# Kernel optimization log

Hardware: AMD Instinct MI355X
Metric: run time of the kernel (lower is better)

The kernel has to match this reference:

```python
import jax, jax.numpy as jnp
import numpy as np

M_MOL = 8192      # number of molecules
A_ATOMS = 32      # atoms per molecule (uniform ragged groups)
N_FEAT = 128      # schnet n_atom_basis


def setup_inputs() -> dict:
    key = jax.random.key(0)
    sr = jax.random.normal(key, (M_MOL * A_ATOMS, N_FEAT), dtype=jnp.float32)
    # idx_m: sorted molecule index per atom, uniform group sizes
    idx_m = jnp.repeat(jnp.arange(M_MOL, dtype=jnp.int32), A_ATOMS)
    return {"scalar_representation": sr, "idx_m": idx_m}


def reference(scalar_representation, idx_m):
    # maxm = int(idx_m[-1]) + 1 in the torch code; groups are uniform here so
    # torch.split over bincount == a simple reshape into [M, A, F].
    maxm = int(idx_m[-1]) + 1
    n_atoms = scalar_representation.shape[0]
    a = n_atoms // maxm
    sr = scalar_representation.reshape(maxm, a, -1)          # [M, A, F]
    # per-molecule correlation (Gram) matrix: c = sr @ sr.T
    c = jnp.einsum('maf,mbf->mab', sr, sr)                    # [M, A, A]
    # eigvalsh returns ascending eigenvalues; torch code takes [0] (smallest)
    eigvals = jnp.linalg.eigvalsh(c)                          # [M, A]
    return eigvals[:, 0]                                      # [M]
```

## Files before the change

### kernel.cpp

```cpp
#include <hip/hip_runtime.h>
#include <hip/hip_bf16.h>

#define DEVINL __device__ __forceinline__

typedef __attribute__((ext_vector_type(8))) short short8;
typedef __attribute__((ext_vector_type(4))) float f32x4;

DEVINL float rcp_f(float x) { return __builtin_amdgcn_rcpf(x); }

#define LDS_FENCE() __asm__ volatile("" ::: "memory")

template<int CTRL>
DEVINL float dpp_mov(float x) {
  return __int_as_float(__builtin_amdgcn_update_dpp(
      0, __float_as_int(x), CTRL, 0xF, 0xF, true));
}
DEVINL float group_sum(float x) {
  x += dpp_mov<0xB1>(x);
  x += dpp_mov<0x4E>(x);
  x += dpp_mov<0x141>(x);
  x += dpp_mov<0x140>(x);
  return x;
}
DEVINL float group_min(float x) {
  x = fminf(x, dpp_mov<0xB1>(x));
  x = fminf(x, dpp_mov<0x4E>(x));
  x = fminf(x, dpp_mov<0x141>(x));
  x = fminf(x, dpp_mov<0x140>(x));
  return x;
}
DEVINL float group_max(float x) {
  x = fmaxf(x, dpp_mov<0xB1>(x));
  x = fmaxf(x, dpp_mov<0x4E>(x));
  x = fmaxf(x, dpp_mov<0x141>(x));
  x = fmaxf(x, dpp_mov<0x140>(x));
  return x;
}

DEVINL short bf_hi(float f, float& rem) {
  unsigned u = __float_as_uint(f);
  unsigned rh = (u + 0x8000u) >> 16;
  rem = f - __uint_as_float(rh << 16);
  return (short)rh;
}
DEVINL short bf_of(float f) {
  return (short)((__float_as_uint(f) + 0x8000u) >> 16);
}
DEVINL void cvt_hilo(float4 fa, float4 fb, short8& h, short8& lo) {
  float rm;
  h[0] = bf_hi(fa.x, rm); lo[0] = bf_of(rm);
  h[1] = bf_hi(fa.y, rm); lo[1] = bf_of(rm);
  h[2] = bf_hi(fa.z, rm); lo[2] = bf_of(rm);
  h[3] = bf_hi(fa.w, rm); lo[3] = bf_of(rm);
  h[4] = bf_hi(fb.x, rm); lo[4] = bf_of(rm);
  h[5] = bf_hi(fb.y, rm); lo[5] = bf_of(rm);
  h[6] = bf_hi(fb.z, rm); lo[6] = bf_of(rm);
  h[7] = bf_hi(fb.w, rm); lo[7] = bf_of(rm);
}
DEVINL f32x4 mfma_bf16(short8 a, short8 b, f32x4 c) {
  return __builtin_amdgcn_mfma_f32_16x16x32_bf16(a, b, c, 0, 0, 0);
}

template<int K>
DEVINL void house_step(float (&r0)[32], float (&r1)[32], int l, int lane,
                       float* vbuf, float* pbuf, float* dbuf, float* ebuf) {
  constexpr int C0 = (K + 1) / 4;

  float xm0, xm1;
  if constexpr (K < 15) xm0 = (l > K) ? r0[K] : 0.0f;
  else                  xm0 = 0.0f;
  if constexpr (K < 16) xm1 = r1[K];
  else                  xm1 = (l > K - 16) ? r1[K] : 0.0f;

  float xsrc = (K + 1 < 16) ? xm0 : xm1;
  float x0 = __shfl(xsrc, (lane & 48) + ((K + 1) & 15), 64);
  float nn = group_sum(xm0 * xm0 + xm1 * xm1);
  float alpha = -copysignf(sqrtf(nn), x0);
  float denom = nn - alpha * x0;
  float beta = (denom > 1e-20f) ? rcp_f(denom) : 0.0f;

  float v0, v1;
  if constexpr (K + 1 < 16) {
    v0 = xm0 - ((l == K + 1) ? alpha : 0.0f);
    v1 = xm1;
  } else {
    v0 = 0.0f;
    v1 = xm1 - ((l == K + 1 - 16) ? alpha : 0.0f);
  }
  vbuf[l] = v0; vbuf[l + 16] = v1;
  LDS_FENCE();

  float4 vc[8];
  #pragma unroll
  for (int c = C0; c < 8; ++c) vc[c] = *(const float4*)(vbuf + 4 * c);

  float p0 = 0.0f;
  if constexpr (K < 15) {
    float a0 = 0.0f, a1 = 0.0f;
    #pragma unroll
    for (int c = C0; c < 8; ++c) {
      a0 = fmaf(r0[4 * c + 0], vc[c].x, a0); a1 = fmaf(r0[4 * c + 1], vc[c].y, a1);
      a0 = fmaf(r0[4 * c + 2], vc[c].z, a0); a1 = fmaf(r0[4 * c + 3], vc[c].w, a1);
    }
    p0 = a0 + a1;
  }
  float b0 = 0.0f, b1 = 0.0f;
  #pragma unroll
  for (int c = C0; c < 8; ++c) {
    b0 = fmaf(r1[4 * c + 0], vc[c].x, b0); b1 = fmaf(r1[4 * c + 1], vc[c].y, b1);
    b0 = fmaf(r1[4 * c + 2], vc[c].z, b0); b1 = fmaf(r1[4 * c + 3], vc[c].w, b1);
  }
  float p1 = b0 + b1;

  pbuf[l] = p0; pbuf[l + 16] = p1;
  LDS_FENCE();
  float G = group_sum(v0 * p0 + v1 * p1);
  float c2 = 0.5f * beta * beta * G;

  float w0 = fmaf(-c2, v0, beta * p0);
  float w1 = fmaf(-c2, v1, beta * p1);

  #pragma unroll
  for (int c = C0; c < 8; ++c) {
    float4 pc = *(const float4*)(pbuf + 4 * c);
    float wx = fmaf(-c2, vc[c].x, beta * pc.x);
    float wy = fmaf(-c2, vc[c].y, beta * pc.y);
    float wz = fmaf(-c2, vc[c].z, beta * pc.z);
    float ww = fmaf(-c2, vc[c].w, beta * pc.w);
    if constexpr (K < 15) {
      r0[4 * c + 0] -= v0 * wx + w0 * vc[c].x;
      r0[4 * c + 1] -= v0 * wy + w0 * vc[c].y;
      r0[4 * c + 2] -= v0 * wz + w0 * vc[c].z;
      r0[4 * c + 3] -= v0 * ww + w0 * vc[c].w;
    }
    r1[4 * c + 0] -= v1 * wx + w1 * vc[c].x;
    r1[4 * c + 1] -= v1 * wy + w1 * vc[c].y;
    r1[4 * c + 2] -= v1 * wz + w1 * vc[c].z;
    r1[4 * c + 3] -= v1 * ww + w1 * vc[c].w;
  }

  if constexpr (K < 16) {
    if (l == K) { dbuf[K] = r0[K]; ebuf[K] = alpha; }
  } else {
    if (l == K - 16) { dbuf[K] = r1[K]; ebuf[K] = alpha; }
  }
}

template<int K>
DEVINL void house_all(float (&r0)[32], float (&r1)[32], int l, int lane,
                      float* vbuf, float* pbuf, float* dbuf, float* ebuf) {
  house_step<K>(r0, r1, l, lane, vbuf, pbuf, dbuf, ebuf);
  if constexpr (K < 30) house_all<K + 1>(r0, r1, l, lane, vbuf, pbuf, dbuf, ebuf);
}

__global__ __launch_bounds__(256) void Correlation_85134841741354_kernel(
    const float* __restrict__ A, float* __restrict__ out, int M) {
  const int lane = threadIdx.x & 63;
  const int wave = threadIdx.x >> 6;
  const int q    = lane >> 4;
  const int t    = lane & 15;
  const int molbase = blockIdx.x * 16 + wave * 4;
  if (molbase >= M) return;

  __shared__ float lds_C[4][32 * 36 + 8];
  __shared__ float ldsv[16][48], ldsp[16][48], ldsd[16][48], ldse[16][48];
  float* Ct   = lds_C[wave];
  const int slot = wave * 4 + q;
  float* vbuf = ldsv[slot];
  float* pbuf = ldsp[slot];
  float* dbuf = ldsd[slot];
  float* ebuf = ldse[slot];

  float r0[32], r1[32];
  #pragma unroll
  for (int m = 0; m < 32; ++m) { r0[m] = 0.0f; r1[m] = 0.0f; }

  #pragma unroll 1
  for (int g = 0; g < 4; ++g) {
    const float* Am = A + (size_t)(molbase + g) * (32 * 128);
    f32x4 acc00 = {0.f, 0.f, 0.f, 0.f}, acc01 = {0.f, 0.f, 0.f, 0.f};
    f32x4 acc10 = {0.f, 0.f, 0.f, 0.f}, acc11 = {0.f, 0.f, 0.f, 0.f};
    #pragma unroll
    for (int c = 0; c < 4; ++c) {
      const float* pr0 = Am + t * 128        + 32 * c + 8 * q;
      const float* pr1 = Am + (t + 16) * 128 + 32 * c + 8 * q;
      float4 fa0 = *(const float4*)(pr0);
      float4 fb0 = *(const float4*)(pr0 + 4);
      float4 fa1 = *(const float4*)(pr1);
      float4 fb1 = *(const float4*)(pr1 + 4);
      short8 h0, l0, h1, l1;
      cvt_hilo(fa0, fb0, h0, l0);
      cvt_hilo(fa1, fb1, h1, l1);
      acc00 = mfma_bf16(h0, h0, acc00); acc00 = mfma_bf16(h0, l0, acc00); acc00 = mfma_bf16(l0, h0, acc00);
      acc01 = mfma_bf16(h0, h1, acc01); acc01 = mfma_bf16(h0, l1, acc01); acc01 = mfma_bf16(l0, h1, acc01);
      acc10 = mfma_bf16(h1, h0, acc10); acc10 = mfma_bf16(h1, l0, acc10); acc10 = mfma_bf16(l1, h0, acc10);
      acc11 = mfma_bf16(h1, h1, acc11); acc11 = mfma_bf16(h1, l1, acc11); acc11 = mfma_bf16(l1, h1, acc11);
    }
    #pragma unroll
    for (int reg = 0; reg < 4; ++reg) {
      Ct[(4 * q + reg) * 36 + t]           = acc00[reg];
      Ct[(4 * q + reg) * 36 + 16 + t]      = acc01[reg];
      Ct[(16 + 4 * q + reg) * 36 + t]      = acc10[reg];
      Ct[(16 + 4 * q + reg) * 36 + 16 + t] = acc11[reg];
    }
    LDS_FENCE();
    if (q == g) {
      #pragma unroll
      for (int c = 0; c < 8; ++c) {
        float4 a = *(const float4*)(Ct + t * 36 + 4 * c);
        r0[4 * c + 0] = a.x; r0[4 * c + 1] = a.y;
        r0[4 * c + 2] = a.z; r0[4 * c + 3] = a.w;
        float4 b = *(const float4*)(Ct + (t + 16) * 36 + 4 * c);
        r1[4 * c + 0] = b.x; r1[4 * c + 1] = b.y;
        r1[4 * c + 2] = b.z; r1[4 * c + 3] = b.w;
      }
    }
    LDS_FENCE();
  }

  house_all<0>(r0, r1, t, lane, vbuf, pbuf, dbuf, ebuf);
  if (t == 15) { dbuf[31] = r1[31]; ebuf[31] = 0.0f; }
  LDS_FENCE();

  float d0 = dbuf[t], d1 = dbuf[t + 16];
  float eh0 = ebuf[t];
  float el0 = (t > 0) ? ebuf[t - 1] : 0.0f;
  float eh1 = ebuf[t + 16];
  float el1 = ebuf[t + 15];
  float rad0 = fabsf(eh0) + fabsf(el0);
  float rad1 = fabsf(eh1) + fabsf(el1);
  float glo = group_min(fminf(d0 - rad0, d1 - rad1));
  float ghi = group_max(fmaxf(d0 + rad0, d1 + rad1));
  float lo = fmaxf(glo - 1e-3f, 0.0f);
  float hi = ghi + 1e-3f;

  float vd[32], ve2[32];
  #pragma unroll
  for (int c = 0; c < 8; ++c) {
    float4 dc = *(const float4*)(dbuf + 4 * c);
    float4 ec = *(const float4*)(ebuf + 4 * c);
    vd[4 * c + 0] = dc.x; vd[4 * c + 1] = dc.y;
    vd[4 * c + 2] = dc.z; vd[4 * c + 3] = dc.w;
    ve2[4 * c + 0] = ec.x * ec.x; ve2[4 * c + 1] = ec.y * ec.y;
    ve2[4 * c + 2] = ec.z * ec.z; ve2[4 * c + 3] = ec.w * ec.w;
  }

  #pragma unroll
  for (int rr = 0; rr < 3; ++rr) {
    float stp = (hi - lo) * (1.0f / 17.0f);
    float sig = fmaf(stp, (float)(t + 1), lo);
    float qq = vd[0] - sig;
    int cnt = (qq < 0.0f) ? 1 : 0;
    #pragma unroll
    for (int i = 1; i < 32; ++i) {
      float qs = (fabsf(qq) < 1e-12f) ? ((qq < 0.0f) ? -1e-12f : 1e-12f) : qq;
      qq = (vd[i] - sig) - ve2[i - 1] * rcp_f(qs);
      cnt += (qq < 0.0f) ? 1 : 0;
    }
    unsigned long long m64 = __ballot(cnt >= 1);
    unsigned hm = (unsigned)((m64 >> (q * 16)) & 0xFFFFu);
    int b = (hm == 0u) ? 16 : (__ffs(hm) - 1);
    float nhi = (b == 16) ? hi : fmaf(stp, (float)(b + 1), lo);
    lo = fmaf(stp, (float)b, lo);
    hi = nhi;
  }

  if (t == 0) out[molbase + q] = 0.5f * (lo + hi);
}

extern "C" void kernel_launch(void* const* d_in, const int* in_sizes, int n_in,
                              void* d_out, int out_size, void* d_ws, size_t ws_size,
                              hipStream_t stream) {
  const float* A = (const float*)d_in[0];
  float* out = (float*)d_out;
  int n_atoms = in_sizes[1];
  int M = n_atoms / 32;
  int blocks = (M + 15) / 16;
  hipLaunchKernelGGL(Correlation_85134841741354_kernel,
                     dim3(blocks), dim3(256), 0, stream, A, out, M);
}
```

Baseline: 213.2 us.

## Overlap Householder vector LDS load with norm reduction and stage all Gram tiles in LDS

Each Householder step now writes the raw column to LDS before the norm reduction, so the vector reload overlaps the DPP sum and alpha is patched into the loaded copy afterwards. The rank-2 update is refactored into per-row scalars so each element costs two FMAs instead of building a w vector. All four Gram matrices per wave are written to distinct LDS tiles and loaded without the per-molecule conditional and fences, and the scratch buffers reuse that tile. LDS use grows to about 73KB per block, which may reduce occupancy.

```diff
diff --git a/kernel.cpp b/kernel.cpp
--- a/kernel.cpp
+++ b/kernel.cpp
@@ -65,6 +65,7 @@
 DEVINL void house_step(float (&r0)[32], float (&r1)[32], int l, int lane,
                        float* vbuf, float* pbuf, float* dbuf, float* ebuf) {
   constexpr int C0 = (K + 1) / 4;
+  constexpr int PE = (K + 1) & 3;
 
   float xm0, xm1;
   if constexpr (K < 15) xm0 = (l > K) ? r0[K] : 0.0f;
@@ -72,9 +73,17 @@
   if constexpr (K < 16) xm1 = r1[K];
   else                  xm1 = (l > K - 16) ? r1[K] : 0.0f;
 
+  vbuf[l] = xm0; vbuf[l + 16] = xm1;
+  LDS_FENCE();
+
   float xsrc = (K + 1 < 16) ? xm0 : xm1;
   float x0 = __shfl(xsrc, (lane & 48) + ((K + 1) & 15), 64);
   float nn = group_sum(xm0 * xm0 + xm1 * xm1);
+
+  float4 vc[8];
+  #pragma unroll
+  for (int c = C0; c < 8; ++c) vc[c] = *(const float4*)(vbuf + 4 * c);
+
   float alpha = -copysignf(sqrtf(nn), x0);
   float denom = nn - alpha * x0;
   float beta = (denom > 1e-20f) ? rcp_f(denom) : 0.0f;
@@ -87,12 +96,10 @@
     v0 = 0.0f;
     v1 = xm1 - ((l == K + 1 - 16) ? alpha : 0.0f);
   }
-  vbuf[l] = v0; vbuf[l + 16] = v1;
-  LDS_FENCE();
-
-  float4 vc[8];
-  #pragma unroll
-  for (int c = C0; c < 8; ++c) vc[c] = *(const float4*)(vbuf + 4 * c);
+  if constexpr (PE == 0)      vc[C0].x -= alpha;
+  else if constexpr (PE == 1) vc[C0].y -= alpha;
+  else if constexpr (PE == 2) vc[C0].z -= alpha;
+  else                        vc[C0].w -= alpha;
 
   float p0 = 0.0f;
   if constexpr (K < 15) {
@@ -117,26 +124,30 @@
   float G = group_sum(v0 * p0 + v1 * p1);
   float c2 = 0.5f * beta * beta * G;
 
-  float w0 = fmaf(-c2, v0, beta * p0);
-  float w1 = fmaf(-c2, v1, beta * p1);
+  float s_p0 = 0.0f, s_v0 = 0.0f;
+  if constexpr (K < 15) {
+    bool act0 = (l > K);
+    s_p0 = beta * v0;
+    s_v0 = act0 ? fmaf(-2.0f * c2, v0, beta * p0) : 0.0f;
+  }
+  float s_p1 = beta * v1;
+  float s_v1;
+  if constexpr (K < 16) s_v1 = fmaf(-2.0f * c2, v1, beta * p1);
+  else                  s_v1 = (l > K - 16) ? fmaf(-2.0f * c2, v1, beta * p1) : 0.0f;
 
   #pragma unroll
   for (int c = C0; c < 8; ++c) {
     float4 pc = *(const float4*)(pbuf + 4 * c);
-    float wx = fmaf(-c2, vc[c].x, beta * pc.x);
-    float wy = fmaf(-c2, vc[c].y, beta * pc.y);
-    float wz = fmaf(-c2, vc[c].z, beta * pc.z);
-    float ww = fmaf(-c2, vc[c].w, beta * pc.w);
     if constexpr (K < 15) {
-      r0[4 * c + 0] -= v0 * wx + w0 * vc[c].x;
-      r0[4 * c + 1] -= v0 * wy + w0 * vc[c].y;
-      r0[4 * c + 2] -= v0 * wz + w0 * vc[c].z;
-      r0[4 * c + 3] -= v0 * ww + w0 * vc[c].w;
-    }
-    r1[4 * c + 0] -= v1 * wx + w1 * vc[c].x;
-    r1[4 * c + 1] -= v1 * wy + w1 * vc[c].y;
-    r1[4 * c + 2] -= v1 * wz + w1 * vc[c].z;
-    r1[4 * c + 3] -= v1 * ww + w1 * vc[c].w;
+      r0[4 * c + 0] -= s_p0 * pc.x + s_v0 * vc[c].x;
+      r0[4 * c + 1] -= s_p0 * pc.y + s_v0 * vc[c].y;
+      r0[4 * c + 2] -= s_p0 * pc.z + s_v0 * vc[c].z;
+      r0[4 * c + 3] -= s_p0 * pc.w + s_v0 * vc[c].w;
+    }
+    r1[4 * c + 0] -= s_p1 * pc.x + s_v1 * vc[c].x;
+    r1[4 * c + 1] -= s_p1 * pc.y + s_v1 * vc[c].y;
+    r1[4 * c + 2] -= s_p1 * pc.z + s_v1 * vc[c].z;
+    r1[4 * c + 3] -= s_p1 * pc.w + s_v1 * vc[c].w;
   }
 
   if constexpr (K < 16) {
@@ -162,18 +173,7 @@
   const int molbase = blockIdx.x * 16 + wave * 4;
   if (molbase >= M) return;
 
-  __shared__ float lds_C[4][32 * 36 + 8];
-  __shared__ float ldsv[16][48], ldsp[16][48], ldsd[16][48], ldse[16][48];
-  float* Ct   = lds_C[wave];
-  const int slot = wave * 4 + q;
-  float* vbuf = ldsv[slot];
-  float* pbuf = ldsp[slot];
-  float* dbuf = ldsd[slot];
-  float* ebuf = ldse[slot];
-
-  float r0[32], r1[32];
-  #pragma unroll
-  for (int m = 0; m < 32; ++m) { r0[m] = 0.0f; r1[m] = 0.0f; }
+  __shared__ float ldsT[4][4][32 * 36 + 8];
 
   #pragma unroll 1
   for (int g = 0; g < 4; ++g) {
@@ -196,27 +196,34 @@
       acc10 = mfma_bf16(h1, h0, acc10); acc10 = mfma_bf16(h1, l0, acc10); acc10 = mfma_bf16(l1, h0, acc10);
       acc11 = mfma_bf16(h1, h1, acc11); acc11 = mfma_bf16(h1, l1, acc11); acc11 = mfma_bf16(l1, h1, acc11);
     }
+    float* tg = &ldsT[wave][g][0];
     #pragma unroll
     for (int reg = 0; reg < 4; ++reg) {
-      Ct[(4 * q + reg) * 36 + t]           = acc00[reg];
-      Ct[(4 * q + reg) * 36 + 16 + t]      = acc01[reg];
-      Ct[(16 + 4 * q + reg) * 36 + t]      = acc10[reg];
-      Ct[(16 + 4 * q + reg) * 36 + 16 + t] = acc11[reg];
-    }
-    LDS_FENCE();
-    if (q == g) {
-      #pragma unroll
-      for (int c = 0; c < 8; ++c) {
-        float4 a = *(const float4*)(Ct + t * 36 + 4 * c);
-        r0[4 * c + 0] = a.x; r0[4 * c + 1] = a.y;
-        r0[4 * c + 2] = a.z; r0[4 * c + 3] = a.w;
-        float4 b = *(const float4*)(Ct + (t + 16) * 36 + 4 * c);
-        r1[4 * c + 0] = b.x; r1[4 * c + 1] = b.y;
-        r1[4 * c + 2] = b.z; r1[4 * c + 3] = b.w;
-      }
-    }
-    LDS_FENCE();
-  }
+      tg[(4 * q + reg) * 36 + t]           = acc00[reg];
+      tg[(4 * q + reg) * 36 + 16 + t]      = acc01[reg];
+      tg[(16 + 4 * q + reg) * 36 + t]      = acc10[reg];
+      tg[(16 + 4 * q + reg) * 36 + 16 + t] = acc11[reg];
+    }
+  }
+  LDS_FENCE();
+
+  float* tq = &ldsT[wave][q][0];
+  float r0[32], r1[32];
+  #pragma unroll
+  for (int c = 0; c < 8; ++c) {
+    float4 a = *(const float4*)(tq + t * 36 + 4 * c);
+    r0[4 * c + 0] = a.x; r0[4 * c + 1] = a.y;
+    r0[4 * c + 2] = a.z; r0[4 * c + 3] = a.w;
+    float4 b = *(const float4*)(tq + (t + 16) * 36 + 4 * c);
+    r1[4 * c + 0] = b.x; r1[4 * c + 1] = b.y;
+    r1[4 * c + 2] = b.z; r1[4 * c + 3] = b.w;
+  }
+  LDS_FENCE();
+
+  float* vbuf = tq;
+  float* pbuf = tq + 40;
+  float* dbuf = tq + 80;
+  float* ebuf = tq + 120;
 
   house_all<0>(r0, r1, t, lane, vbuf, pbuf, dbuf, ebuf);
   if (t == 15) { dbuf[31] = r1[31]; ebuf[31] = 0.0f; }
```

Result: faster. 208.6 us (-2.1%).
